# Kernel tuning notes

Measured on AMD Instinct MI355X. Metric: run time of the kernel, lower is better.

The kernel has to match this reference:

```python
import jax, jax.numpy as jnp
import numpy as np

V, MAXLEN, D, FF, H, L = 50257, 1024, 768, 3072, 12, 12
HD = D // H


def _ln(x, w, b, eps=1e-5):
    mu = jnp.mean(x, axis=-1, keepdims=True)
    var = jnp.var(x, axis=-1, keepdims=True)
    return (x - mu) * jax.lax.rsqrt(var + eps) * w + b


def setup_inputs() -> dict:
    key = jax.random.key(0)
    ks = jax.random.split(key, 16)
    s = 0.02
    inp = {
        "tokens": jax.random.randint(ks[0], (2, 1024), 0, V),
        "tok_embed": jax.random.normal(ks[1], (V, D), jnp.float32) * s,
        "pos_embed": jax.random.normal(ks[2], (MAXLEN, D), jnp.float32) * s,
        # stacked per-layer params, weights stored [in, out]
        "qkv_w": jax.random.normal(ks[3], (L, D, 3 * D), jnp.float32) * s,
        "qkv_b": jnp.zeros((L, 3 * D), jnp.float32),
        "proj_w": jax.random.normal(ks[4], (L, D, D), jnp.float32) * s,
        "proj_b": jnp.zeros((L, D), jnp.float32),
        "ln1_w": jnp.ones((L, D), jnp.float32),
        "ln1_b": jnp.zeros((L, D), jnp.float32),
        "ln2_w": jnp.ones((L, D), jnp.float32),
        "ln2_b": jnp.zeros((L, D), jnp.float32),
        "fc1_w": jax.random.normal(ks[5], (L, D, FF), jnp.float32) * s,
        "fc1_b": jnp.zeros((L, FF), jnp.float32),
        "fc2_w": jax.random.normal(ks[6], (L, FF, D), jnp.float32) * s,
        "fc2_b": jnp.zeros((L, D), jnp.float32),
        "lnf_w": jnp.ones((D,), jnp.float32),
        "lnf_b": jnp.zeros((D,), jnp.float32),
    }
    return inp


def _gpt2(tokens, tok_embed, pos_embed, qkv_w, qkv_b, proj_w, proj_b,
          ln1_w, ln1_b, ln2_w, ln2_b, fc1_w, fc1_b, fc2_w, fc2_b, lnf_w, lnf_b):
    B, T = tokens.shape
    x = tok_embed[tokens] + pos_embed[jnp.arange(T)][None, :, :]  # [B,T,D]
    causal = jnp.tril(jnp.ones((T, T), bool))[None, None]          # [1,1,T,T]
    neg = jnp.finfo(x.dtype).min

    def block(x, p):
        (qw, qb, pw, pb, l1w, l1b, l2w, l2b, f1w, f1b, f2w, f2b) = p
        h = _ln(x, l1w, l1b)
        qkv = h @ qw + qb                                          # [B,T,3D]
        q, k, v = jnp.split(qkv, 3, axis=-1)
        q = q.reshape(B, T, H, HD).transpose(0, 2, 1, 3)           # [B,H,T,HD]
        k = k.reshape(B, T, H, HD).transpose(0, 2, 1, 3)
        v = v.reshape(B, T, H, HD).transpose(0, 2, 1, 3)
        att = jnp.einsum('bhqd,bhkd->bhqk', q, k) / np.sqrt(HD).astype(x.dtype)
        att = jnp.where(causal, att, neg)
        att = jax.nn.softmax(att, axis=-1)
        o = jnp.einsum('bhqk,bhkd->bhqd', att, v)
        o = o.transpose(0, 2, 1, 3).reshape(B, T, D)
        x = x + o @ pw + pb
        h2 = _ln(x, l2w, l2b)
        ff = jax.nn.gelu(h2 @ f1w + f1b, approximate=True) @ f2w + f2b
        return x + ff, None

    params = (qkv_w, qkv_b, proj_w, proj_b, ln1_w, ln1_b, ln2_w, ln2_b,
              fc1_w, fc1_b, fc2_w, fc2_b)
    x, _ = jax.lax.scan(block, x, params)
    x = _ln(x, lnf_w, lnf_b)
    return x @ tok_embed.T                                         # tied lm_head [B,T,V]


def reference(tokens, tok_embed, pos_embed, qkv_w, qkv_b, proj_w, proj_b,
              ln1_w, ln1_b, ln2_w, ln2_b, fc1_w, fc1_b, fc2_w, fc2_b,
              lnf_w, lnf_b):
    return _gpt2(tokens, tok_embed, pos_embed, qkv_w, qkv_b, proj_w, proj_b,
                 ln1_w, ln1_b, ln2_w, ln2_b, fc1_w, fc1_b, fc2_w, fc2_b,
                 lnf_w, lnf_b)
```

## Files before the change

### kernel.cpp

```cpp
#include <hip/hip_runtime.h>

#define TT 1024
#define DD 768
#define FFD 3072
#define NH 12
#define NL 12
#define HDIM 64
#define VOC 50257
#define BT 2048

typedef __attribute__((ext_vector_type(8))) __bf16 bf16x8;
typedef __attribute__((ext_vector_type(4))) float f32x4;
typedef __attribute__((ext_vector_type(4))) unsigned short u16x4;
typedef unsigned short u16;

static __device__ __forceinline__ u16 f2bf(float f) {
  unsigned int u = __float_as_uint(f);
  u += 0x7FFF + ((u >> 16) & 1);
  return (u16)(u >> 16);
}

static __device__ __forceinline__ void load_lds16(const u16* g, u16* l) {
  __builtin_amdgcn_global_load_lds(
      (const __attribute__((address_space(1))) unsigned int*)g,
      (__attribute__((address_space(3))) unsigned int*)l, 16, 0, 0);
}

__global__ __launch_bounds__(256) void transpose_convert(
    const float* __restrict__ in, u16* __restrict__ out, int R, int C) {
  __shared__ float tile[32][33];
  const long long zo = (long long)blockIdx.z * R * C;
  const int c0 = blockIdx.x * 32, r0 = blockIdx.y * 32;
  const int tx = threadIdx.x & 31, ty = threadIdx.x >> 5;
#pragma unroll
  for (int i = 0; i < 32; i += 8)
    tile[ty + i][tx] = in[zo + (long long)(r0 + ty + i) * C + c0 + tx];
  __syncthreads();
#pragma unroll
  for (int i = 0; i < 32; i += 8)
    out[zo + (long long)(c0 + ty + i) * R + r0 + tx] = f2bf(tile[tx][ty + i]);
}

__global__ void convert_bf16(const float* __restrict__ in, u16* __restrict__ out,
                             long long n) {
  long long i = (long long)blockIdx.x * 256 + threadIdx.x;
  const long long stride = (long long)gridDim.x * 256;
  for (; i < n; i += stride) out[i] = f2bf(in[i]);
}

__global__ __launch_bounds__(256) void embed_kernel(
    const int* __restrict__ tokens, const float* __restrict__ tokE,
    const float* __restrict__ posE, float* __restrict__ x) {
  const int row = blockIdx.x;
  const int t = row & (TT - 1);
  const int tok = tokens[row];
  const int tid = threadIdx.x;
#pragma unroll
  for (int c = 0; c < 3; ++c) {
    int d = tid + c * 256;
    x[(long long)row * DD + d] = tokE[(long long)tok * DD + d] + posE[(long long)t * DD + d];
  }
}

__global__ __launch_bounds__(256) void ln_sum(
    float* __restrict__ x, const float* __restrict__ pp, int nsum,
    const float* __restrict__ w, const float* __restrict__ b,
    u16* __restrict__ out) {
  const int row = blockIdx.x;
  const long long base = (long long)row * DD;
  const int tid = threadIdx.x;
  float v[3];
  float s = 0.f, s2 = 0.f;
#pragma unroll
  for (int c = 0; c < 3; ++c) {
    const int d = tid + c * 256;
    float t = x[base + d];
    for (int q = 0; q < nsum; ++q) t += pp[(long long)q * BT * DD + base + d];
    if (nsum) x[base + d] = t;
    v[c] = t; s += t; s2 += t * t;
  }
  for (int off = 32; off; off >>= 1) {
    s += __shfl_down(s, off, 64);
    s2 += __shfl_down(s2, off, 64);
  }
  __shared__ float rs[8];
  if ((tid & 63) == 0) { rs[tid >> 6] = s; rs[4 + (tid >> 6)] = s2; }
  __syncthreads();
  s = rs[0] + rs[1] + rs[2] + rs[3];
  s2 = rs[4] + rs[5] + rs[6] + rs[7];
  const float mu = s * (1.0f / DD);
  const float var = s2 * (1.0f / DD) - mu * mu;
  const float inv = rsqrtf(var + 1e-5f);
  u16* o = out + base;
#pragma unroll
  for (int c = 0; c < 3; ++c) {
    int d = tid + c * 256;
    o[d] = f2bf((v[c] - mu) * inv * w[d] + b[d]);
  }
}

__global__ __launch_bounds__(256, 3) void flash_attn(
    const u16* __restrict__ qkv, const u16* __restrict__ vT,
    u16* __restrict__ attn) {
  __shared__ __align__(16) u16 Qs[64 * 64];
  __shared__ __align__(16) u16 Ks0[64 * 64];
  __shared__ __align__(16) u16 Ks1[64 * 64];
  __shared__ __align__(16) u16 Vs0[64 * 64];
  __shared__ __align__(16) u16 Vs1[64 * 64];
  __shared__ __align__(16) u16 Ps[4 * 16 * 72];

  const int id = blockIdx.x;
  const int qt = 15 - id / 24;
  const int z = id % 24;
  const int b = z / NH, h = z - (z / NH) * NH;
  const int q0 = qt * 64;

  const int tid = threadIdx.x;
  const int lane = tid & 63;
  const int wave = __builtin_amdgcn_readfirstlane(tid >> 6);
  const int mf = lane & 15;
  const int quad = lane >> 4;

  const int srow = wave * 16 + (lane >> 3);
  const int srow1 = srow + 8;
  const int sch0 = (((lane & 7) ^ ((srow >> 1) & 7))) * 8;
  const int sch1 = (((lane & 7) ^ ((srow1 >> 1) & 7))) * 8;
  const int lb = wave * 1024;

  const u16* qk_base = qkv + (long long)b * TT * 2304 + h * 64;

  auto stageKV = [&](u16* Kd, u16* Vd, int kv0) {
    load_lds16(qk_base + (long long)(kv0 + srow) * 2304 + 768 + sch0, Kd + lb);
    load_lds16(qk_base + (long long)(kv0 + srow1) * 2304 + 768 + sch1, Kd + lb + 512);
    load_lds16(vT + (long long)(z * 64 + srow) * 1024 + kv0 + sch0, Vd + lb);
    load_lds16(vT + (long long)(z * 64 + srow1) * 1024 + kv0 + sch1, Vd + lb + 512);
  };

  load_lds16(qk_base + (long long)(q0 + srow) * 2304 + sch0, Qs + lb);
  load_lds16(qk_base + (long long)(q0 + srow1) * 2304 + sch1, Qs + lb + 512);
  stageKV(Ks0, Vs0, 0);
  __syncthreads();

  bf16x8 qfr[2];
  {
    const int r = wave * 16 + mf;
    const int sw = (r >> 1) & 7;
#pragma unroll
    for (int ks = 0; ks < 2; ++ks)
      qfr[ks] = *(const bf16x8*)(Qs + r * 64 + (((ks * 4 + quad) ^ sw) * 8));
  }

  f32x4 oacc[4] = {};
  float mrun = -1e30f, lrun = 0.f;
  u16 *Kc = Ks0, *Vc = Vs0, *Kn = Ks1, *Vn = Vs1;

  for (int t = 0; t <= qt; ++t) {
    if (t < qt) stageKV(Kn, Vn, (t + 1) * 64);
    const int diag = (t == qt);

    f32x4 sacc[4] = {};
#pragma unroll
    for (int ks = 0; ks < 2; ++ks)
#pragma unroll
      for (int i = 0; i < 4; ++i) {
        const int r = i * 16 + mf;
        bf16x8 kfr = *(const bf16x8*)(Kc + r * 64 + (((ks * 4 + quad) ^ ((r >> 1) & 7)) * 8));
        sacc[i] = __builtin_amdgcn_mfma_f32_16x16x32_bf16(kfr, qfr[ks], sacc[i], 0, 0, 0);
      }

    float pv[4][4];
    float tmax = -1e30f;
#pragma unroll
    for (int i = 0; i < 4; ++i)
#pragma unroll
      for (int r = 0; r < 4; ++r) {
        float v = sacc[i][r] * 0.125f;
        if (diag) {
          const int kvl = i * 16 + quad * 4 + r;
          if (kvl > wave * 16 + mf) v = -1e30f;
        }
        pv[i][r] = v;
        tmax = fmaxf(tmax, v);
      }
    tmax = fmaxf(tmax, __shfl_xor(tmax, 16, 64));
    tmax = fmaxf(tmax, __shfl_xor(tmax, 32, 64));
    const float mnew = fmaxf(mrun, tmax);
    const float fac = __expf(mrun - mnew);
    float lsum = 0.f;
#pragma unroll
    for (int i = 0; i < 4; ++i)
#pragma unroll
      for (int r = 0; r < 4; ++r) {
        float e = __expf(pv[i][r] - mnew);
        pv[i][r] = e;
        lsum += e;
      }
    lsum += __shfl_xor(lsum, 16, 64);
    lsum += __shfl_xor(lsum, 32, 64);
    lrun = lrun * fac + lsum;
    mrun = mnew;

    float fo[4];
#pragma unroll
    for (int r = 0; r < 4; ++r) fo[r] = __shfl(fac, (lane & 48) | (quad * 4 + r), 64);
#pragma unroll
    for (int j = 0; j < 4; ++j)
#pragma unroll
      for (int r = 0; r < 4; ++r) oacc[j][r] *= fo[r];

#pragma unroll
    for (int i = 0; i < 4; ++i) {
      u16x4 pk;
#pragma unroll
      for (int r = 0; r < 4; ++r) pk[r] = f2bf(pv[i][r]);
      *(u16x4*)(Ps + wave * 1152 + mf * 72 + i * 16 + quad * 4) = pk;
    }
#pragma unroll
    for (int ks = 0; ks < 2; ++ks) {
      bf16x8 pfr = *(const bf16x8*)(Ps + wave * 1152 + mf * 72 + ks * 32 + quad * 8);
#pragma unroll
      for (int j = 0; j < 4; ++j) {
        const int r = j * 16 + mf;
        bf16x8 vfr = *(const bf16x8*)(Vc + r * 64 + (((ks * 4 + quad) ^ ((r >> 1) & 7)) * 8));
        oacc[j] = __builtin_amdgcn_mfma_f32_16x16x32_bf16(pfr, vfr, oacc[j], 0, 0, 0);
      }
    }
    __syncthreads();
    u16* tk = Kc; Kc = Kn; Kn = tk;
    u16* tv = Vc; Vc = Vn; Vn = tv;
  }

  const float linv = 1.0f / lrun;
  float li[4];
#pragma unroll
  for (int r = 0; r < 4; ++r) li[r] = __shfl(linv, (lane & 48) | (quad * 4 + r), 64);
#pragma unroll
  for (int j = 0; j < 4; ++j)
#pragma unroll
    for (int r = 0; r < 4; ++r) {
      const int q = q0 + wave * 16 + quad * 4 + r;
      const int d = j * 16 + mf;
      attn[(long long)(b * TT + q) * 768 + h * 64 + d] = f2bf(oacc[j][r] * li[r]);
    }
}

enum { EPI_F32 = 0, EPI_BF16_BIAS = 1, EPI_BF16_BIAS_GELU = 2,
       EPI_BF16 = 4, EPI_QKV = 5, EPI_SPLITK_PART = 6 };

template <int EPI, int BM = 128>
__global__ __launch_bounds__(256, BM == 256 ? 2 : 3) void gemm_nt(
    const u16* __restrict__ A, const u16* __restrict__ Bm,
    const float* __restrict__ bias,
    void* __restrict__ Cout, u16* __restrict__ vtAux,
    int M, int N, int K, int lda, int ldb, int ldc,
    long long aHi, long long aLo, long long bHi, long long bLo,
    long long cHi, long long cLo, int Hdiv, int swapxy,
    int xcdChunk, int kSplit) {
  constexpr int AISS = BM / 64;
  constexpr int MI = BM / 32;
  __shared__ __align__(16) u16 As0[BM * 32];
  __shared__ __align__(16) u16 As1[BM * 32];
  __shared__ __align__(16) u16 Bs0[128 * 32];
  __shared__ __align__(16) u16 Bs1[128 * 32];
  const int z = blockIdx.z;
  int zb = 0, zh = 0;
  long long koff = 0;
  if (kSplit > 1) {
    const int slice = K / kSplit;
    koff = (long long)z * slice;
    K = slice;
  } else {
    zb = z / Hdiv; zh = z - zb * Hdiv;
  }
  const u16* Ab = A + zb * aHi + zh * aLo + koff;
  const u16* Bb = Bm + zb * bHi + zh * bLo + koff;
  const long long cOff = (long long)zb * cHi + (long long)zh * cLo;

  int rx = blockIdx.x, ry = blockIdx.y;
  if (xcdChunk) {
    const int id = ry * gridDim.x + rx;
    const int w = (id & 7) * xcdChunk + (id >> 3);
    rx = w % gridDim.x;
    ry = w / gridDim.x;
  }
  const int bx = swapxy ? ry : rx;
  const int by = swapxy ? rx : ry;
  const int m0 = by * BM;
  const int n0 = bx * 128;

  const int tid = threadIdx.x;
  const int lane = tid & 63;
  const int wave = __builtin_amdgcn_readfirstlane(tid >> 6);
  const int wm = (wave >> 1) * (BM / 2);
  const int wn = (wave & 1) * 64;
  const int mf = lane & 15;
  const int quad = lane >> 4;

  const u16* agp[AISS];
#pragma unroll
  for (int i = 0; i < AISS; ++i) {
    const int r = wave * (BM / 4) + i * 16 + (lane >> 2);
    const int c = ((lane & 3) ^ ((r >> 1) & 3)) * 8;
    agp[i] = Ab + (long long)(m0 + r) * lda + c;
  }
  const int sr0 = wave * 32 + (lane >> 2);
  const int sr1 = sr0 + 16;
  const int sc0 = ((lane & 3) ^ ((sr0 >> 1) & 3)) * 8;
  const int sc1 = ((lane & 3) ^ ((sr1 >> 1) & 3)) * 8;
  int br0 = n0 + sr0; if (br0 >= N) br0 = N - 1;
  int br1 = n0 + sr1; if (br1 >= N) br1 = N - 1;
  const u16* bgp0 = Bb + (long long)br0 * ldb + sc0;
  const u16* bgp1 = Bb + (long long)br1 * ldb + sc1;
  const int aoffW = wave * (BM * 8);
  const int woff = wave * 1024;

  auto stage = [&](u16* Ad, u16* Bd, int kk) {
#pragma unroll
    for (int i = 0; i < AISS; ++i) load_lds16(agp[i] + kk, Ad + aoffW + i * 512);
    load_lds16(bgp0 + kk, Bd + woff);
    load_lds16(bgp1 + kk, Bd + woff + 512);
  };

  int aoff[MI], boff[4];
#pragma unroll
  for (int i = 0; i < MI; ++i) {
    const int ar = wm + i * 16 + mf;
    aoff[i] = ar * 32 + ((quad ^ ((ar >> 1) & 3)) * 8);
  }
#pragma unroll
  for (int j = 0; j < 4; ++j) {
    const int br = wn + j * 16 + mf;
    boff[j] = br * 32 + ((quad ^ ((br >> 1) & 3)) * 8);
  }

  f32x4 acc[MI][4] = {};

  auto compute = [&](const u16* Asb, const u16* Bsb) {
    bf16x8 afr[MI], bfr[4];
#pragma unroll
    for (int i = 0; i < MI; ++i) afr[i] = *(const bf16x8*)(Asb + aoff[i]);
#pragma unroll
    for (int j = 0; j < 4; ++j) bfr[j] = *(const bf16x8*)(Bsb + boff[j]);
#pragma unroll
    for (int i = 0; i < MI; ++i)
#pragma unroll
      for (int j = 0; j < 4; ++j)
        acc[i][j] = __builtin_amdgcn_mfma_f32_16x16x32_bf16(afr[i], bfr[j], acc[i][j], 0, 0, 0);
  };

  stage(As0, Bs0, 0);
  __syncthreads();
  for (int k0 = 0; k0 < K; k0 += 64) {
    if (k0 + 32 < K) stage(As1, Bs1, k0 + 32);
    compute(As0, Bs0);
    __syncthreads();
    if (k0 + 64 < K) stage(As0, Bs0, k0 + 64);
    compute(As1, Bs1);
    __syncthreads();
  }

#pragma unroll
  for (int j = 0; j < 4; ++j) {
    const int col = n0 + wn + j * 16 + mf;
    if (col >= N) continue;
    float bv = 0.0f;
    if (EPI == EPI_BF16_BIAS || EPI == EPI_BF16_BIAS_GELU || EPI == EPI_QKV)
      bv = bias[col];
    if (EPI == EPI_SPLITK_PART && z == 0) bv = bias[col];
    if (EPI == EPI_QKV && col >= 1536) {
      const int hd = col - 1536;
#pragma unroll
      for (int i = 0; i < MI; ++i) {
        const int t0 = m0 + wm + i * 16 + quad * 4;
        u16x4 pk;
#pragma unroll
        for (int r = 0; r < 4; ++r) pk[r] = f2bf(acc[i][j][r] + bv);
        const int b_ = t0 >> 10;
        const long long vi =
            ((long long)((b_ * NH + (hd >> 6)) * 64 + (hd & 63))) * 1024 + (t0 & 1023);
        *(u16x4*)(vtAux + vi) = pk;
      }
      continue;
    }
#pragma unroll
    for (int i = 0; i < MI; ++i) {
#pragma unroll
      for (int r = 0; r < 4; ++r) {
        const int row = m0 + wm + i * 16 + quad * 4 + r;
        float v = acc[i][j][r] + bv;
        if (EPI == EPI_BF16_BIAS_GELU) {
          float u = v + 0.044715f * v * v * v;
          v = 0.5f * v * (1.0f + tanhf(0.7978845608028654f * u));
        }
        if (EPI == EPI_SPLITK_PART) {
          ((float*)Cout)[(long long)z * M * ldc + (long long)row * ldc + col] = v;
        } else {
          const long long ci = cOff + (long long)row * ldc + col;
          if (EPI == EPI_F32) {
            ((float*)Cout)[ci] = v;
          } else {
            ((u16*)Cout)[ci] = f2bf(v);
          }
        }
      }
    }
  }
}

extern "C" void kernel_launch(void* const* d_in, const int* in_sizes, int n_in,
                              void* d_out, int out_size, void* d_ws, size_t ws_size,
                              hipStream_t stream) {
  const int* tokens      = (const int*)d_in[0];
  const float* tok_embed = (const float*)d_in[1];
  const float* pos_embed = (const float*)d_in[2];
  const float* qkv_w     = (const float*)d_in[3];
  const float* qkv_b     = (const float*)d_in[4];
  const float* proj_w    = (const float*)d_in[5];
  const float* proj_b    = (const float*)d_in[6];
  const float* ln1_w     = (const float*)d_in[7];
  const float* ln1_b     = (const float*)d_in[8];
  const float* ln2_w     = (const float*)d_in[9];
  const float* ln2_b     = (const float*)d_in[10];
  const float* fc1_w     = (const float*)d_in[11];
  const float* fc1_b     = (const float*)d_in[12];
  const float* fc2_w     = (const float*)d_in[13];
  const float* fc2_b     = (const float*)d_in[14];
  const float* lnf_w     = (const float*)d_in[15];
  const float* lnf_b     = (const float*)d_in[16];

  if (ws_size < 440u * 1024u * 1024u) return;

  char* p = (char*)d_ws;
  auto alloc = [&](size_t bytes) {
    void* r = (void*)p;
    p += (bytes + 255) & ~(size_t)255;
    return r;
  };
  u16* wq   = (u16*)alloc((size_t)NL * 2304 * 768 * 2);
  u16* wp   = (u16*)alloc((size_t)NL * 768 * 768 * 2);
  u16* w1   = (u16*)alloc((size_t)NL * 3072 * 768 * 2);
  u16* w2   = (u16*)alloc((size_t)NL * 768 * 3072 * 2);
  u16* te   = (u16*)alloc((size_t)VOC * 768 * 2);
  float* x  = (float*)alloc((size_t)BT * 768 * 4);
  u16* hbuf = (u16*)alloc((size_t)BT * 768 * 2);
  u16* qkv  = (u16*)alloc((size_t)BT * 2304 * 2);
  u16* vT   = (u16*)alloc((size_t)24 * 64 * 1024 * 2);
  u16* attn = (u16*)alloc((size_t)BT * 768 * 2);
  u16* ff   = (u16*)alloc((size_t)BT * 3072 * 2);
  u16* xf   = (u16*)alloc((size_t)BT * 768 * 2);
  float* pp = (float*)alloc((size_t)4 * BT * 768 * 4);

  transpose_convert<<<dim3(2304 / 32, 768 / 32, NL), 256, 0, stream>>>(qkv_w, wq, 768, 2304);
  transpose_convert<<<dim3(768 / 32, 768 / 32, NL), 256, 0, stream>>>(proj_w, wp, 768, 768);
  transpose_convert<<<dim3(3072 / 32, 768 / 32, NL), 256, 0, stream>>>(fc1_w, w1, 768, 3072);
  transpose_convert<<<dim3(768 / 32, 3072 / 32, NL), 256, 0, stream>>>(fc2_w, w2, 3072, 768);
  convert_bf16<<<4096, 256, 0, stream>>>(tok_embed, te, (long long)VOC * 768);
  embed_kernel<<<BT, 256, 0, stream>>>(tokens, tok_embed, pos_embed, x);

  for (int l = 0; l < NL; ++l) {
    ln_sum<<<BT, 256, 0, stream>>>(x, pp, l == 0 ? 0 : 4,
                                   ln1_w + l * 768, ln1_b + l * 768, hbuf);
    gemm_nt<EPI_QKV><<<dim3(2304 / 128, BT / 128, 1), 256, 0, stream>>>(
        hbuf, wq + (size_t)l * 2304 * 768, qkv_b + l * 2304, qkv, vT,
        BT, 2304, 768, 768, 768, 2304, 0, 0, 0, 0, 0, 0, 1, 0, 288 / 8, 1);
    flash_attn<<<384, 256, 0, stream>>>(qkv, vT, attn);
    gemm_nt<EPI_SPLITK_PART><<<dim3(768 / 128, BT / 128, 2), 256, 0, stream>>>(
        attn, wp + (size_t)l * 768 * 768, proj_b + l * 768, pp, nullptr,
        BT, 768, 768, 768, 768, 768, 0, 0, 0, 0, 0, 0, 1, 0, 96 / 8, 2);
    ln_sum<<<BT, 256, 0, stream>>>(x, pp, 2,
                                   ln2_w + l * 768, ln2_b + l * 768, hbuf);
    gemm_nt<EPI_BF16_BIAS_GELU><<<dim3(3072 / 128, BT / 128, 1), 256, 0, stream>>>(
        hbuf, w1 + (size_t)l * 3072 * 768, fc1_b + l * 3072, ff, nullptr,
        BT, 3072, 768, 768, 768, 3072, 0, 0, 0, 0, 0, 0, 1, 0, 384 / 8, 1);
    gemm_nt<EPI_SPLITK_PART><<<dim3(768 / 128, BT / 128, 4), 256, 0, stream>>>(
        ff, w2 + (size_t)l * 768 * 3072, fc2_b + l * 768, pp, nullptr,
        BT, 768, 3072, 3072, 3072, 768, 0, 0, 0, 0, 0, 0, 1, 0, 96 / 8, 4);
  }
  ln_sum<<<BT, 256, 0, stream>>>(x, pp, 4, lnf_w, lnf_b, xf);
  gemm_nt<EPI_F32, 256><<<dim3(BT / 256, (VOC + 127) / 128, 1), 256, 0, stream>>>(
      xf, te, nullptr, (float*)d_out, nullptr,
      BT, VOC, 768, 768, 768, VOC, 0, 0, 0, 0, 0, 0, 1, 1, 3144 / 8, 1);
}
```

Before: 2.531 ms.

## Drop BM=256 tile, use nontemporal logit stores, split proj GEMM three ways

```diff
diff --git a/kernel.cpp b/kernel.cpp
--- a/kernel.cpp
+++ b/kernel.cpp
@@ -247,8 +247,8 @@
 enum { EPI_F32 = 0, EPI_BF16_BIAS = 1, EPI_BF16_BIAS_GELU = 2,
        EPI_BF16 = 4, EPI_QKV = 5, EPI_SPLITK_PART = 6 };
 
-template <int EPI, int BM = 128>
-__global__ __launch_bounds__(256, BM == 256 ? 2 : 3) void gemm_nt(
+template <int EPI>
+__global__ __launch_bounds__(256, 3) void gemm_nt(
     const u16* __restrict__ A, const u16* __restrict__ Bm,
     const float* __restrict__ bias,
     void* __restrict__ Cout, u16* __restrict__ vtAux,
@@ -256,10 +256,8 @@
     long long aHi, long long aLo, long long bHi, long long bLo,
     long long cHi, long long cLo, int Hdiv, int swapxy,
     int xcdChunk, int kSplit) {
-  constexpr int AISS = BM / 64;
-  constexpr int MI = BM / 32;
-  __shared__ __align__(16) u16 As0[BM * 32];
-  __shared__ __align__(16) u16 As1[BM * 32];
+  __shared__ __align__(16) u16 As0[128 * 32];
+  __shared__ __align__(16) u16 As1[128 * 32];
   __shared__ __align__(16) u16 Bs0[128 * 32];
   __shared__ __align__(16) u16 Bs1[128 * 32];
   const int z = blockIdx.z;
@@ -285,64 +283,55 @@
   }
   const int bx = swapxy ? ry : rx;
   const int by = swapxy ? rx : ry;
-  const int m0 = by * BM;
+  const int m0 = by * 128;
   const int n0 = bx * 128;
 
   const int tid = threadIdx.x;
   const int lane = tid & 63;
   const int wave = __builtin_amdgcn_readfirstlane(tid >> 6);
-  const int wm = (wave >> 1) * (BM / 2);
+  const int wm = (wave >> 1) * 64;
   const int wn = (wave & 1) * 64;
   const int mf = lane & 15;
   const int quad = lane >> 4;
 
-  const u16* agp[AISS];
-#pragma unroll
-  for (int i = 0; i < AISS; ++i) {
-    const int r = wave * (BM / 4) + i * 16 + (lane >> 2);
-    const int c = ((lane & 3) ^ ((r >> 1) & 3)) * 8;
-    agp[i] = Ab + (long long)(m0 + r) * lda + c;
-  }
   const int sr0 = wave * 32 + (lane >> 2);
   const int sr1 = sr0 + 16;
   const int sc0 = ((lane & 3) ^ ((sr0 >> 1) & 3)) * 8;
   const int sc1 = ((lane & 3) ^ ((sr1 >> 1) & 3)) * 8;
   int br0 = n0 + sr0; if (br0 >= N) br0 = N - 1;
   int br1 = n0 + sr1; if (br1 >= N) br1 = N - 1;
+  const u16* agp0 = Ab + (long long)(m0 + sr0) * lda + sc0;
+  const u16* agp1 = Ab + (long long)(m0 + sr1) * lda + sc1;
   const u16* bgp0 = Bb + (long long)br0 * ldb + sc0;
   const u16* bgp1 = Bb + (long long)br1 * ldb + sc1;
-  const int aoffW = wave * (BM * 8);
   const int woff = wave * 1024;
 
   auto stage = [&](u16* Ad, u16* Bd, int kk) {
-#pragma unroll
-    for (int i = 0; i < AISS; ++i) load_lds16(agp[i] + kk, Ad + aoffW + i * 512);
+    load_lds16(agp0 + kk, Ad + woff);
+    load_lds16(agp1 + kk, Ad + woff + 512);
     load_lds16(bgp0 + kk, Bd + woff);
     load_lds16(bgp1 + kk, Bd + woff + 512);
   };
 
-  int aoff[MI], boff[4];
-#pragma unroll
-  for (int i = 0; i < MI; ++i) {
+  int aoff[4], boff[4];
+#pragma unroll
+  for (int i = 0; i < 4; ++i) {
     const int ar = wm + i * 16 + mf;
     aoff[i] = ar * 32 + ((quad ^ ((ar >> 1) & 3)) * 8);
-  }
-#pragma unroll
-  for (int j = 0; j < 4; ++j) {
-    const int br = wn + j * 16 + mf;
-    boff[j] = br * 32 + ((quad ^ ((br >> 1) & 3)) * 8);
-  }
-
-  f32x4 acc[MI][4] = {};
+    const int br = wn + i * 16 + mf;
+    boff[i] = br * 32 + ((quad ^ ((br >> 1) & 3)) * 8);
+  }
+
+  f32x4 acc[4][4] = {};
 
   auto compute = [&](const u16* Asb, const u16* Bsb) {
-    bf16x8 afr[MI], bfr[4];
-#pragma unroll
-    for (int i = 0; i < MI; ++i) afr[i] = *(const bf16x8*)(Asb + aoff[i]);
+    bf16x8 afr[4], bfr[4];
+#pragma unroll
+    for (int i = 0; i < 4; ++i) afr[i] = *(const bf16x8*)(Asb + aoff[i]);
 #pragma unroll
     for (int j = 0; j < 4; ++j) bfr[j] = *(const bf16x8*)(Bsb + boff[j]);
 #pragma unroll
-    for (int i = 0; i < MI; ++i)
+    for (int i = 0; i < 4; ++i)
 #pragma unroll
       for (int j = 0; j < 4; ++j)
         acc[i][j] = __builtin_amdgcn_mfma_f32_16x16x32_bf16(afr[i], bfr[j], acc[i][j], 0, 0, 0);
@@ -370,7 +359,7 @@
     if (EPI == EPI_QKV && col >= 1536) {
       const int hd = col - 1536;
 #pragma unroll
-      for (int i = 0; i < MI; ++i) {
+      for (int i = 0; i < 4; ++i) {
         const int t0 = m0 + wm + i * 16 + quad * 4;
         u16x4 pk;
 #pragma unroll
@@ -383,7 +372,7 @@
       continue;
     }
 #pragma unroll
-    for (int i = 0; i < MI; ++i) {
+    for (int i = 0; i < 4; ++i) {
 #pragma unroll
       for (int r = 0; r < 4; ++r) {
         const int row = m0 + wm + i * 16 + quad * 4 + r;
@@ -397,7 +386,7 @@
         } else {
           const long long ci = cOff + (long long)row * ldc + col;
           if (EPI == EPI_F32) {
-            ((float*)Cout)[ci] = v;
+            __builtin_nontemporal_store(v, (float*)Cout + ci);
           } else {
             ((u16*)Cout)[ci] = f2bf(v);
           }
@@ -464,10 +453,10 @@
         hbuf, wq + (size_t)l * 2304 * 768, qkv_b + l * 2304, qkv, vT,
         BT, 2304, 768, 768, 768, 2304, 0, 0, 0, 0, 0, 0, 1, 0, 288 / 8, 1);
     flash_attn<<<384, 256, 0, stream>>>(qkv, vT, attn);
-    gemm_nt<EPI_SPLITK_PART><<<dim3(768 / 128, BT / 128, 2), 256, 0, stream>>>(
+    gemm_nt<EPI_SPLITK_PART><<<dim3(768 / 128, BT / 128, 3), 256, 0, stream>>>(
         attn, wp + (size_t)l * 768 * 768, proj_b + l * 768, pp, nullptr,
-        BT, 768, 768, 768, 768, 768, 0, 0, 0, 0, 0, 0, 1, 0, 96 / 8, 2);
-    ln_sum<<<BT, 256, 0, stream>>>(x, pp, 2,
+        BT, 768, 768, 768, 768, 768, 0, 0, 0, 0, 0, 0, 1, 0, 96 / 8, 3);
+    ln_sum<<<BT, 256, 0, stream>>>(x, pp, 3,
                                    ln2_w + l * 768, ln2_b + l * 768, hbuf);
     gemm_nt<EPI_BF16_BIAS_GELU><<<dim3(3072 / 128, BT / 128, 1), 256, 0, stream>>>(
         hbuf, w1 + (size_t)l * 3072 * 768, fc1_b + l * 3072, ff, nullptr,
@@ -477,7 +466,7 @@
         BT, 768, 3072, 3072, 3072, 768, 0, 0, 0, 0, 0, 0, 1, 0, 96 / 8, 4);
   }
   ln_sum<<<BT, 256, 0, stream>>>(x, pp, 4, lnf_w, lnf_b, xf);
-  gemm_nt<EPI_F32, 256><<<dim3(BT / 256, (VOC + 127) / 128, 1), 256, 0, stream>>>(
+  gemm_nt<EPI_F32><<<dim3(BT / 128, (VOC + 127) / 128, 1), 256, 0, stream>>>(
       xf, te, nullptr, (float*)d_out, nullptr,
-      BT, VOC, 768, 768, 768, VOC, 0, 0, 0, 0, 0, 0, 1, 1, 3144 / 8, 1);
-}
+      BT, VOC, 768, 768, 768, VOC, 0, 0, 0, 0, 0, 0, 1, 1, 6288 / 8, 1);
+}
```

Measured after the change: 2.695 ms. 6.5% more time.
